# Kernel optimization log

Hardware: AMD Instinct MI355X
Metric: run time of the kernel (lower is better)

## Reference

```python
import jax, jax.numpy as jnp
import numpy as np
from jax import lax

B, L = 64, 262144


def setup_inputs() -> dict:
    key = jax.random.key(0)
    kx, kr, kth, kb = jax.random.split(key, 4)
    x = jax.random.normal(kx, (B, L), dtype=jnp.float32)
    # Stable denominator: poles at radius r in [0, 0.95], angle th in [0, pi]
    # a1 = -2 r cos(th), a2 = r^2  (docstring: stability enforced by caller)
    r = jax.random.uniform(kr, (B,), minval=0.0, maxval=0.95)
    th = jax.random.uniform(kth, (B,), minval=0.0, maxval=np.pi)
    a1 = -2.0 * r * jnp.cos(th)
    a2 = r * r
    bcoef = jax.random.normal(kb, (B, 3), dtype=jnp.float32) * 0.5
    coeffs = jnp.concatenate([bcoef, a1[:, None], a2[:, None]], axis=1).astype(jnp.float32)  # (B,5)
    return {"x": x, "coeffs": coeffs}


def reference(x, coeffs):
    # x: (B, L), coeffs: (B, 5) = [b0, b1, b2, a1, a2]
    if coeffs.ndim == 1:
        coeffs = jnp.broadcast_to(coeffs[None, :], (x.shape[0], 5))
    b0, b1, b2, a1, a2 = (coeffs[:, i] for i in range(5))
    s0 = jnp.zeros(x.shape[0], dtype=x.dtype)

    def step(carry, xn):
        s1, s2 = carry
        yn = b0 * xn + s1                 # direct form II transposed
        s1n = b1 * xn - a1 * yn + s2
        s2n = b2 * xn - a2 * yn
        return (s1n, s2n), yn

    _, ys = lax.scan(step, (s0, s0), x.T)  # scan over L; ys: (L, B)
    return ys.T
```

## Files before the change

### kernel.cpp

```cpp
#include <hip/hip_runtime.h>


constexpr int B_DIM = 64;
constexpr int L_DIM = 262144;
constexpr int K = 32;
constexpr int CPR = L_DIM / K;
constexpr int OC = 56;
constexpr int WPR = (CPR + OC - 1) / OC;
constexpr int TOTAL_WAVES = B_DIM * WPR;
constexpr int T = 256;
constexpr int WPB = T / 64;
constexpr int GRID = TOTAL_WAVES / WPB;
constexpr int RS = 9;
constexpr int ROWS = 64;
constexpr int WAVE_LDS = ROWS * RS;
constexpr int ROW_F4 = L_DIM / 4;

#define BIQ_STEP(xs)                                            \
    do {                                                        \
        float yv_ = fmaf(b0, (xs), s1);                         \
        float t1_ = fmaf(b1, (xs), s2);                         \
        s2 = fmaf(-a2, yv_, b2 * (xs));                         \
        s1 = fmaf(-a1, yv_, t1_);                               \
    } while (0)

#define BIQ_STEP_Y(xs, yd)                                      \
    do {                                                        \
        (yd) = fmaf(b0, (xs), s1);                              \
        float t1_ = fmaf(b1, (xs), s2);                         \
        s2 = fmaf(-a2, (yd), b2 * (xs));                        \
        s1 = fmaf(-a1, (yd), t1_);                              \
    } while (0)

__global__ __launch_bounds__(T) void biquad_wavescan3(
    const float* __restrict__ x,
    const float* __restrict__ coeffs,
    float* __restrict__ y)
{
    __shared__ float4 lds[WPB * WAVE_LDS];

    const int gtid = blockIdx.x * T + threadIdx.x;
    const int gw   = gtid >> 6;
    const int lane = gtid & 63;
    const int row  = gw / WPR;
    const int w    = gw - row * WPR;
    const int c    = w * OC - 8 + lane;

    float4* wlds = &lds[(threadIdx.x >> 6) * WAVE_LDS];

    const float4* xrow = (const float4*)(x + (size_t)row * L_DIM);
    const int rbase = (w * OC - 8) * (K / 4);
    #pragma unroll
    for (int j = 0; j < 8; ++j) {
        int f = j * 64 + lane;
        int src = rbase + f;
        src = src < 0 ? 0 : (src >= ROW_F4 ? ROW_F4 - 1 : src);
        wlds[(f >> 3) * RS + (f & 7)] = xrow[src];
    }

    const float* cf = coeffs + row * 5;
    const float b0 = cf[0], b1 = cf[1], b2 = cf[2];
    const float a1 = cf[3], a2 = cf[4];

    const bool active = (c >= 0) && (c < CPR);

    float4 xv[8];
    {
        const float4* rp = &wlds[lane * RS];
        #pragma unroll
        for (int j = 0; j < 8; ++j) xv[j] = rp[j];
    }

    float s1 = 0.f, s2 = 0.f;
    #pragma unroll
    for (int i = 0; i < 8; ++i) {
        BIQ_STEP(xv[i].x); BIQ_STEP(xv[i].y); BIQ_STEP(xv[i].z); BIQ_STEP(xv[i].w);
    }

    float p00 = -a1, p01 = 1.f, p10 = -a2, p11 = 0.f;
    #pragma unroll
    for (int i = 0; i < 5; ++i) {
        float q00 = fmaf(p00, p00, p01 * p10);
        float q01 = fmaf(p00, p01, p01 * p11);
        float q10 = fmaf(p10, p00, p11 * p10);
        float q11 = fmaf(p10, p01, p11 * p11);
        p00 = q00; p01 = q01; p10 = q10; p11 = q11;
    }

    float f1 = active ? s1 : 0.f;
    float f2 = active ? s2 : 0.f;
    if (!active) { p00 = 1.f; p01 = 0.f; p10 = 0.f; p11 = 1.f; }

    #pragma unroll
    for (int d = 1; d < 64; d <<= 1) {
        float q00 = __shfl_up(p00, d, 64);
        float q01 = __shfl_up(p01, d, 64);
        float q10 = __shfl_up(p10, d, 64);
        float q11 = __shfl_up(p11, d, 64);
        float g1  = __shfl_up(f1,  d, 64);
        float g2  = __shfl_up(f2,  d, 64);
        if (lane >= d) {
            float n00 = fmaf(p00, q00, p01 * q10);
            float n01 = fmaf(p00, q01, p01 * q11);
            float n10 = fmaf(p10, q00, p11 * q10);
            float n11 = fmaf(p10, q01, p11 * q11);
            f1 = fmaf(p00, g1, fmaf(p01, g2, f1));
            f2 = fmaf(p10, g1, fmaf(p11, g2, f2));
            p00 = n00; p01 = n01; p10 = n10; p11 = n11;
        }
    }

    float e1 = __shfl_up(f1, 1, 64);
    float e2 = __shfl_up(f2, 1, 64);

    if (lane >= 8 && c < CPR) {
        s1 = e1; s2 = e2;
        float4* wp = &wlds[lane * RS];
        #pragma unroll
        for (int i = 0; i < 8; ++i) {
            float4 yv;
            BIQ_STEP_Y(xv[i].x, yv.x);
            BIQ_STEP_Y(xv[i].y, yv.y);
            BIQ_STEP_Y(xv[i].z, yv.z);
            BIQ_STEP_Y(xv[i].w, yv.w);
            wp[i] = yv;
        }
    }

    const int first = w * OC;
    int nvalid = CPR - first; if (nvalid > OC) nvalid = OC;
    float4* ydst = (float4*)(y + (size_t)row * L_DIM) + first * (K / 4);
    for (int g = lane; g < nvalid * 8; g += 64) {
        ydst[g] = wlds[((g >> 3) + 8) * RS + (g & 7)];
    }
}

extern "C" void kernel_launch(void* const* d_in, const int* in_sizes, int n_in,
                              void* d_out, int out_size, void* d_ws, size_t ws_size,
                              hipStream_t stream) {
    const float* x      = (const float*)d_in[0];
    const float* coeffs = (const float*)d_in[1];
    float*       yout   = (float*)d_out;

    biquad_wavescan3<<<GRID, T, 0, stream>>>(x, coeffs, yout);
}
```

Before: 112.7 us.

## Process two regions per wave with register prefetch and XOR-swizzled LDS

Each wave now handles two consecutive chunk regions instead of one, and the grid is halved to match. The global loads for the second region are issued into registers before the first region is computed, so their latency can overlap with the scan work. The LDS tile drops its padded stride of 9 in favour of an XOR swizzle. Inputs are re-read from LDS in both passes instead of being held in registers, which lowers register pressure but adds LDS traffic and halves the number of waves available to hide latency.

Result: slower. 137.7 us (+22.1%).

```diff
diff --git a/kernel.cpp b/kernel.cpp
--- a/kernel.cpp
+++ b/kernel.cpp
@@ -7,14 +7,13 @@
 constexpr int CPR = L_DIM / K;
 constexpr int OC = 56;
 constexpr int WPR = (CPR + OC - 1) / OC;
-constexpr int TOTAL_WAVES = B_DIM * WPR;
+constexpr int REGIONS = B_DIM * WPR;
 constexpr int T = 256;
 constexpr int WPB = T / 64;
-constexpr int GRID = TOTAL_WAVES / WPB;
-constexpr int RS = 9;
-constexpr int ROWS = 64;
-constexpr int WAVE_LDS = ROWS * RS;
+constexpr int NW = REGIONS / 2;
+constexpr int GRID = NW / WPB;
 constexpr int ROW_F4 = L_DIM / 4;
+constexpr int WLDS = 512;
 
 #define BIQ_STEP(xs)                                            \
     do {                                                        \
@@ -32,107 +31,130 @@
         s1 = fmaf(-a1, (yd), t1_);                              \
     } while (0)
 
-__global__ __launch_bounds__(T) void biquad_wavescan3(
+__global__ __launch_bounds__(T) void biquad_pipe(
     const float* __restrict__ x,
     const float* __restrict__ coeffs,
     float* __restrict__ y)
 {
-    __shared__ float4 lds[WPB * WAVE_LDS];
+    __shared__ float4 lds[WPB * WLDS];
 
     const int gtid = blockIdx.x * T + threadIdx.x;
     const int gw   = gtid >> 6;
     const int lane = gtid & 63;
-    const int row  = gw / WPR;
-    const int w    = gw - row * WPR;
-    const int c    = w * OC - 8 + lane;
+    float4* wlds = &lds[(threadIdx.x >> 6) * WLDS];
+    const int lx   = lane & 7;
+    const int lrow = lane * 8;
 
-    float4* wlds = &lds[(threadIdx.x >> 6) * WAVE_LDS];
+    float4 nxt[8];
 
-    const float4* xrow = (const float4*)(x + (size_t)row * L_DIM);
-    const int rbase = (w * OC - 8) * (K / 4);
-    #pragma unroll
-    for (int j = 0; j < 8; ++j) {
-        int f = j * 64 + lane;
-        int src = rbase + f;
-        src = src < 0 ? 0 : (src >= ROW_F4 ? ROW_F4 - 1 : src);
-        wlds[(f >> 3) * RS + (f & 7)] = xrow[src];
-    }
+    auto prefetch = [&](int rg) {
+        const int row = rg / WPR;
+        const int w   = rg - row * WPR;
+        const float4* xrow = (const float4*)(x + (size_t)row * L_DIM);
+        const int rbase = (w * OC - 8) * (K / 4);
+        #pragma unroll
+        for (int j = 0; j < 8; ++j) {
+            int s = rbase + j * 64 + lane;
+            s = s < 0 ? 0 : (s >= ROW_F4 ? ROW_F4 - 1 : s);
+            nxt[j] = xrow[s];
+        }
+    };
 
-    const float* cf = coeffs + row * 5;
-    const float b0 = cf[0], b1 = cf[1], b2 = cf[2];
-    const float a1 = cf[3], a2 = cf[4];
+    auto stage = [&]() {
+        #pragma unroll
+        for (int j = 0; j < 8; ++j) {
+            const int f = j * 64 + lane;
+            const int r = f >> 3;
+            wlds[r * 8 + ((f & 7) ^ (r & 7))] = nxt[j];
+        }
+    };
 
-    const bool active = (c >= 0) && (c < CPR);
+    auto process = [&](int rg) {
+        const int row = rg / WPR;
+        const int w   = rg - row * WPR;
+        const int c   = w * OC - 8 + lane;
 
-    float4 xv[8];
-    {
-        const float4* rp = &wlds[lane * RS];
+        const float* cf = coeffs + row * 5;
+        const float b0 = cf[0], b1 = cf[1], b2 = cf[2];
+        const float a1 = cf[3], a2 = cf[4];
+        const bool active = (c >= 0) && (c < CPR);
+
+        float s1 = 0.f, s2 = 0.f;
         #pragma unroll
-        for (int j = 0; j < 8; ++j) xv[j] = rp[j];
-    }
+        for (int j = 0; j < 8; ++j) {
+            float4 xv = wlds[lrow + (j ^ lx)];
+            BIQ_STEP(xv.x); BIQ_STEP(xv.y); BIQ_STEP(xv.z); BIQ_STEP(xv.w);
+        }
 
-    float s1 = 0.f, s2 = 0.f;
-    #pragma unroll
-    for (int i = 0; i < 8; ++i) {
-        BIQ_STEP(xv[i].x); BIQ_STEP(xv[i].y); BIQ_STEP(xv[i].z); BIQ_STEP(xv[i].w);
-    }
+        float p00 = -a1, p01 = 1.f, p10 = -a2, p11 = 0.f;
+        #pragma unroll
+        for (int i = 0; i < 5; ++i) {
+            float q00 = fmaf(p00, p00, p01 * p10);
+            float q01 = fmaf(p00, p01, p01 * p11);
+            float q10 = fmaf(p10, p00, p11 * p10);
+            float q11 = fmaf(p10, p01, p11 * p11);
+            p00 = q00; p01 = q01; p10 = q10; p11 = q11;
+        }
 
-    float p00 = -a1, p01 = 1.f, p10 = -a2, p11 = 0.f;
-    #pragma unroll
-    for (int i = 0; i < 5; ++i) {
-        float q00 = fmaf(p00, p00, p01 * p10);
-        float q01 = fmaf(p00, p01, p01 * p11);
-        float q10 = fmaf(p10, p00, p11 * p10);
-        float q11 = fmaf(p10, p01, p11 * p11);
-        p00 = q00; p01 = q01; p10 = q10; p11 = q11;
-    }
+        float f1 = active ? s1 : 0.f;
+        float f2 = active ? s2 : 0.f;
+        if (!active) { p00 = 1.f; p01 = 0.f; p10 = 0.f; p11 = 1.f; }
 
-    float f1 = active ? s1 : 0.f;
-    float f2 = active ? s2 : 0.f;
-    if (!active) { p00 = 1.f; p01 = 0.f; p10 = 0.f; p11 = 1.f; }
+        #pragma unroll
+        for (int d = 1; d < 64; d <<= 1) {
+            float q00 = __shfl_up(p00, d, 64);
+            float q01 = __shfl_up(p01, d, 64);
+            float q10 = __shfl_up(p10, d, 64);
+            float q11 = __shfl_up(p11, d, 64);
+            float g1  = __shfl_up(f1,  d, 64);
+            float g2  = __shfl_up(f2,  d, 64);
+            if (lane >= d) {
+                float n00 = fmaf(p00, q00, p01 * q10);
+                float n01 = fmaf(p00, q01, p01 * q11);
+                float n10 = fmaf(p10, q00, p11 * q10);
+                float n11 = fmaf(p10, q01, p11 * q11);
+                f1 = fmaf(p00, g1, fmaf(p01, g2, f1));
+                f2 = fmaf(p10, g1, fmaf(p11, g2, f2));
+                p00 = n00; p01 = n01; p10 = n10; p11 = n11;
+            }
+        }
 
-    #pragma unroll
-    for (int d = 1; d < 64; d <<= 1) {
-        float q00 = __shfl_up(p00, d, 64);
-        float q01 = __shfl_up(p01, d, 64);
-        float q10 = __shfl_up(p10, d, 64);
-        float q11 = __shfl_up(p11, d, 64);
-        float g1  = __shfl_up(f1,  d, 64);
-        float g2  = __shfl_up(f2,  d, 64);
-        if (lane >= d) {
-            float n00 = fmaf(p00, q00, p01 * q10);
-            float n01 = fmaf(p00, q01, p01 * q11);
-            float n10 = fmaf(p10, q00, p11 * q10);
-            float n11 = fmaf(p10, q01, p11 * q11);
-            f1 = fmaf(p00, g1, fmaf(p01, g2, f1));
-            f2 = fmaf(p10, g1, fmaf(p11, g2, f2));
-            p00 = n00; p01 = n01; p10 = n10; p11 = n11;
+        float e1 = __shfl_up(f1, 1, 64);
+        float e2 = __shfl_up(f2, 1, 64);
+
+        if (lane >= 8 && c < CPR) {
+            s1 = e1; s2 = e2;
+            #pragma unroll
+            for (int j = 0; j < 8; ++j) {
+                const int idx = lrow + (j ^ lx);
+                float4 xv = wlds[idx];
+                float4 yv;
+                BIQ_STEP_Y(xv.x, yv.x);
+                BIQ_STEP_Y(xv.y, yv.y);
+                BIQ_STEP_Y(xv.z, yv.z);
+                BIQ_STEP_Y(xv.w, yv.w);
+                wlds[idx] = yv;
+            }
         }
-    }
 
-    float e1 = __shfl_up(f1, 1, 64);
-    float e2 = __shfl_up(f2, 1, 64);
+        const int first = w * OC;
+        int nvalid = CPR - first; if (nvalid > OC) nvalid = OC;
+        float4* ydst = (float4*)(y + (size_t)row * L_DIM) + first * (K / 4);
+        for (int g = lane; g < nvalid * 8; g += 64) {
+            const int r = (g >> 3) + 8;
+            ydst[g] = wlds[r * 8 + ((g & 7) ^ (r & 7))];
+        }
+    };
 
-    if (lane >= 8 && c < CPR) {
-        s1 = e1; s2 = e2;
-        float4* wp = &wlds[lane * RS];
-        #pragma unroll
-        for (int i = 0; i < 8; ++i) {
-            float4 yv;
-            BIQ_STEP_Y(xv[i].x, yv.x);
-            BIQ_STEP_Y(xv[i].y, yv.y);
-            BIQ_STEP_Y(xv[i].z, yv.z);
-            BIQ_STEP_Y(xv[i].w, yv.w);
-            wp[i] = yv;
-        }
-    }
+    const int rgA = 2 * gw;
+    const int rgB = 2 * gw + 1;
 
-    const int first = w * OC;
-    int nvalid = CPR - first; if (nvalid > OC) nvalid = OC;
-    float4* ydst = (float4*)(y + (size_t)row * L_DIM) + first * (K / 4);
-    for (int g = lane; g < nvalid * 8; g += 64) {
-        ydst[g] = wlds[((g >> 3) + 8) * RS + (g & 7)];
-    }
+    prefetch(rgA);
+    stage();
+    prefetch(rgB);
+    process(rgA);
+    stage();
+    process(rgB);
 }
 
 extern "C" void kernel_launch(void* const* d_in, const int* in_sizes, int n_in,
@@ -142,5 +164,5 @@
     const float* coeffs = (const float*)d_in[1];
     float*       yout   = (float*)d_out;
 
-    biquad_wavescan3<<<GRID, T, 0, stream>>>(x, coeffs, yout);
+    biquad_pipe<<<GRID, T, 0, stream>>>(x, coeffs, yout);
 }
```
